# Performance work log

Hardware: AMD Instinct MI355X
Metric: run time of the kernel (lower is better)

Reference implementation:

```python
import jax, jax.numpy as jnp
import numpy as np


def _sobel_kernels(dtype):
    # kornia sobel order=1, normalized: divide by sum(|k|)=8
    gx = jnp.array([[-1., 0., 1.], [-2., 0., 2.], [-1., 0., 1.]], dtype=dtype) / 8.0
    gy = gx.T
    return jnp.stack([gx, gy])[:, None]  # (2, 1, 3, 3) OIHW


def _spatial_gradient(x):
    # x: (b, c, h, w) -> gx, gy each (b, c, h, w)
    b, c, h, w = x.shape
    xp = jnp.pad(x.reshape(b * c, 1, h, w), ((0, 0), (0, 0), (1, 1), (1, 1)), mode='edge')
    k = _sobel_kernels(x.dtype)
    out = jax.lax.conv_general_dilated(
        xp, k, window_strides=(1, 1), padding='VALID',
        dimension_numbers=('NCHW', 'OIHW', 'NCHW'))  # (b*c, 2, h, w)
    out = out.reshape(b, c, 2, h, w)
    return out[:, :, 0], out[:, :, 1]


def setup_inputs() -> dict:
    key = jax.random.key(0)
    x = jax.random.normal(key, (16, 3, 512, 512), dtype=jnp.float32)
    return {"x": x}


def reference(x):
    b, c, h, w = x.shape
    gx, gy = _spatial_gradient(x)  # (b, c, h, w) each
    if c == 3:
        mag_c = jnp.sqrt(gx * gx + gy * gy + 1e-9)  # per-channel magnitude
        # first-occurrence argmax over channels matches torch .max(dim) tie-break
        idx = jnp.argmax(mag_c, axis=1)  # (b, h, w)
        gxs = jnp.take_along_axis(gx, idx[:, None], axis=1)[:, 0]  # (b, h, w)
        gys = jnp.take_along_axis(gy, idx[:, None], axis=1)[:, 0]
    else:
        gxs, gys = gx, gy
    magnitude = jnp.sqrt(gxs * gxs + gys * gys + 1e-9)
    # clipped_div(gx, gy, 10.0)
    y_tr = jnp.where(gys == 0.0, jnp.asarray(1e-9, gys.dtype), gys)
    angle = jnp.clip(gxs / y_tr, -10.0, 10.0)
    return magnitude, angle
```

## Files before the change

### kernel.cpp

```cpp
#include <hip/hip_runtime.h>


constexpr int Hc = 512;
constexpr int Wc = 512;
constexpr int Cc = 3;

__global__ __launch_bounds__(256, 8) void sobel_mag_angle_kernel(
    const float* __restrict__ x, float* __restrict__ out, int B) {
    int tid = blockIdx.x * 256 + threadIdx.x;
    int l  = tid & 127;
    int w0 = l << 2;

    int h = __builtin_amdgcn_readfirstlane((tid >> 7) & (Hc - 1));
    int b = __builtin_amdgcn_readfirstlane(tid >> 16);
    int rm = (h == 0) ? 0 : h - 1;
    int rp = (h + 1 < Hc) ? h + 1 : Hc - 1;

    int wl = (w0 == 0) ? 0 : w0 - 1;
    int wr = (w0 + 4 < Wc) ? w0 + 4 : Wc - 1;

    const float* xb = x + (size_t)b * (Cc * Hc * Wc);

    float bm[4], bgx[4], bgy[4];

#pragma unroll
    for (int c = 0; c < Cc; ++c) {
        const float* base = xb + c * (Hc * Wc);
        const float* p0 = base + rm * Wc;
        const float* p1 = base + h * Wc;
        const float* p2 = base + rp * Wc;

        float col[3][6];
        {
            float4 v0 = *(const float4*)(p0 + w0);
            float4 v1 = *(const float4*)(p1 + w0);
            float4 v2 = *(const float4*)(p2 + w0);
            float L0 = p0[wl], R0 = p0[wr];
            float L1 = p1[wl], R1 = p1[wr];
            float L2 = p2[wl], R2 = p2[wr];
            col[0][0] = L0; col[0][1] = v0.x; col[0][2] = v0.y; col[0][3] = v0.z; col[0][4] = v0.w; col[0][5] = R0;
            col[1][0] = L1; col[1][1] = v1.x; col[1][2] = v1.y; col[1][3] = v1.z; col[1][4] = v1.w; col[1][5] = R1;
            col[2][0] = L2; col[2][1] = v2.x; col[2][2] = v2.y; col[2][3] = v2.z; col[2][4] = v2.w; col[2][5] = R2;
        }
#pragma unroll
        for (int i = 0; i < 4; ++i) {
            float t0 = col[0][i + 2] - col[0][i];
            float t1 = col[1][i + 2] - col[1][i];
            float t2 = col[2][i + 2] - col[2][i];
            float gx = 0.125f * (t0 + t2) + 0.25f * t1;
            float u0 = col[2][i]     - col[0][i];
            float u1 = col[2][i + 1] - col[0][i + 1];
            float u2 = col[2][i + 2] - col[0][i + 2];
            float gy = 0.125f * (u0 + u2) + 0.25f * u1;
            float m = __builtin_amdgcn_sqrtf(gx * gx + gy * gy + 1e-9f);
            if (c == 0) {
                bm[i] = m; bgx[i] = gx; bgy[i] = gy;
            } else {
                bool gt = m > bm[i];
                bm[i]  = gt ? m  : bm[i];
                bgx[i] = gt ? gx : bgx[i];
                bgy[i] = gt ? gy : bgy[i];
            }
        }
    }

    float mo[4], ao[4];
#pragma unroll
    for (int i = 0; i < 4; ++i) {
        mo[i] = bm[i];
        float yt = (bgy[i] == 0.0f) ? 1e-9f : bgy[i];
        float a = bgx[i] * __builtin_amdgcn_rcpf(yt);
        ao[i] = fminf(fmaxf(a, -10.0f), 10.0f);
    }

    size_t npix = (size_t)B * (Hc * Wc);
    size_t obase = ((size_t)b * Hc + h) * Wc;
    float* po = out + obase;
    *(float4*)(po + w0)        = make_float4(mo[0], mo[1], mo[2], mo[3]);
    *(float4*)(po + npix + w0) = make_float4(ao[0], ao[1], ao[2], ao[3]);
}

extern "C" void kernel_launch(void* const* d_in, const int* in_sizes, int n_in,
                              void* d_out, int out_size, void* d_ws, size_t ws_size,
                              hipStream_t stream) {
    const float* x = (const float*)d_in[0];
    float* out = (float*)d_out;
    int B = in_sizes[0] / (Cc * Hc * Wc);
    int total_threads = B * Hc * (Wc / 4);
    int blocks = total_threads / 256;
    sobel_mag_angle_kernel<<<blocks, 256, 0, stream>>>(x, out, B);
}
```

Measured before the change: 102.7 us.

## Stage row tiles with halo in LDS via direct global-to-LDS loads

Each block now covers a 4-row strip of one image. It loads 6 rows × 3 channels into shared memory with global_load_lds, so vertically adjacent output rows reuse the same input rows from LDS instead of each re-reading three rows from global memory. Each thread then computes 8 pixels of one row from LDS. The aim is to cut redundant global and L2 traffic. The cost is 36KB of LDS per block, lower occupancy, and a full wait plus barrier before any compute, with no overlap of load and compute.

```diff
diff --git a/kernel.cpp b/kernel.cpp
--- a/kernel.cpp
+++ b/kernel.cpp
@@ -1,56 +1,71 @@
 #include <hip/hip_runtime.h>
+#include <stdint.h>
 
 
 constexpr int Hc = 512;
 constexpr int Wc = 512;
 constexpr int Cc = 3;
+constexpr int RT = 4;
+constexpr int TR = RT + 2;
 
-__global__ __launch_bounds__(256, 8) void sobel_mag_angle_kernel(
+__global__ __launch_bounds__(256, 4) void sobel_mag_angle_kernel(
     const float* __restrict__ x, float* __restrict__ out, int B) {
-    int tid = blockIdx.x * 256 + threadIdx.x;
-    int l  = tid & 127;
-    int w0 = l << 2;
+    __shared__ float lds[Cc * TR * Wc];
 
-    int h = __builtin_amdgcn_readfirstlane((tid >> 7) & (Hc - 1));
-    int b = __builtin_amdgcn_readfirstlane(tid >> 16);
-    int rm = (h == 0) ? 0 : h - 1;
-    int rp = (h + 1 < Hc) ? h + 1 : Hc - 1;
+    int bid = blockIdx.x;
+    int b  = bid >> 7;
+    int h0 = (bid & 127) * RT;
 
-    int wl = (w0 == 0) ? 0 : w0 - 1;
-    int wr = (w0 + 4 < Wc) ? w0 + 4 : Wc - 1;
+    int t = threadIdx.x;
+    int wave = t >> 6;
+    int lane = t & 63;
 
     const float* xb = x + (size_t)b * (Cc * Hc * Wc);
+#pragma unroll
+    for (int s2 = 0; s2 < 9; ++s2) {
+        int s = wave * 9 + s2;
+        int ch = s / 12;
+        int rr = (s % 12) >> 1;
+        int half = s & 1;
+        int srow = h0 + rr - 1;
+        srow = srow < 0 ? 0 : (srow > Hc - 1 ? Hc - 1 : srow);
+        const float* gp = xb + ((size_t)ch * Hc + srow) * Wc + half * 256 + lane * 4;
+        float* lp = &lds[(ch * TR + rr) * Wc + half * 256];
+        __builtin_amdgcn_global_load_lds(
+            (const __attribute__((address_space(1))) void*)gp,
+            (__attribute__((address_space(3))) void*)lp, 16, 0, 0);
+    }
+    asm volatile("s_waitcnt vmcnt(0)" ::: "memory");
+    __syncthreads();
 
-    float bm[4], bgx[4], bgy[4];
+    int r = wave;
+    int w0 = lane << 3;
+    int wl = (w0 == 0) ? 0 : w0 - 1;
+    int wr = (w0 + 8 < Wc) ? w0 + 8 : Wc - 1;
 
+    float bm[8], bgx[8], bgy[8];
 #pragma unroll
     for (int c = 0; c < Cc; ++c) {
-        const float* base = xb + c * (Hc * Wc);
-        const float* p0 = base + rm * Wc;
-        const float* p1 = base + h * Wc;
-        const float* p2 = base + rp * Wc;
-
-        float col[3][6];
-        {
-            float4 v0 = *(const float4*)(p0 + w0);
-            float4 v1 = *(const float4*)(p1 + w0);
-            float4 v2 = *(const float4*)(p2 + w0);
-            float L0 = p0[wl], R0 = p0[wr];
-            float L1 = p1[wl], R1 = p1[wr];
-            float L2 = p2[wl], R2 = p2[wr];
-            col[0][0] = L0; col[0][1] = v0.x; col[0][2] = v0.y; col[0][3] = v0.z; col[0][4] = v0.w; col[0][5] = R0;
-            col[1][0] = L1; col[1][1] = v1.x; col[1][2] = v1.y; col[1][3] = v1.z; col[1][4] = v1.w; col[1][5] = R1;
-            col[2][0] = L2; col[2][1] = v2.x; col[2][2] = v2.y; col[2][3] = v2.z; col[2][4] = v2.w; col[2][5] = R2;
+        float row[3][10];
+#pragma unroll
+        for (int k = 0; k < 3; ++k) {
+            const float* lrow = &lds[(c * TR + (r + k)) * Wc];
+            float4 A  = *(const float4*)(lrow + w0);
+            float4 Bv = *(const float4*)(lrow + w0 + 4);
+            row[k][0] = lrow[wl];
+            row[k][1] = A.x;  row[k][2] = A.y;  row[k][3] = A.z;  row[k][4] = A.w;
+            row[k][5] = Bv.x; row[k][6] = Bv.y; row[k][7] = Bv.z; row[k][8] = Bv.w;
+            row[k][9] = lrow[wr];
         }
 #pragma unroll
-        for (int i = 0; i < 4; ++i) {
-            float t0 = col[0][i + 2] - col[0][i];
-            float t1 = col[1][i + 2] - col[1][i];
-            float t2 = col[2][i + 2] - col[2][i];
+        for (int i = 0; i < 8; ++i) {
+            float t0 = row[0][i + 2] - row[0][i];
+            float t1 = row[1][i + 2] - row[1][i];
+            float t2 = row[2][i + 2] - row[2][i];
             float gx = 0.125f * (t0 + t2) + 0.25f * t1;
-            float u0 = col[2][i]     - col[0][i];
-            float u1 = col[2][i + 1] - col[0][i + 1];
-            float u2 = col[2][i + 2] - col[0][i + 2];
+            float u0 = row[2][i]     - row[0][i];
+            float u1 = row[2][i + 1] - row[0][i + 1];
+            float u2 = row[2][i + 2] - row[0][i + 2];
             float gy = 0.125f * (u0 + u2) + 0.25f * u1;
             float m = __builtin_amdgcn_sqrtf(gx * gx + gy * gy + 1e-9f);
             if (c == 0) {
@@ -64,9 +79,9 @@
         }
     }
 
-    float mo[4], ao[4];
+    float mo[8], ao[8];
 #pragma unroll
-    for (int i = 0; i < 4; ++i) {
+    for (int i = 0; i < 8; ++i) {
         mo[i] = bm[i];
         float yt = (bgy[i] == 0.0f) ? 1e-9f : bgy[i];
         float a = bgx[i] * __builtin_amdgcn_rcpf(yt);
@@ -74,10 +89,12 @@
     }
 
     size_t npix = (size_t)B * (Hc * Wc);
-    size_t obase = ((size_t)b * Hc + h) * Wc;
+    size_t obase = ((size_t)b * Hc + (h0 + r)) * Wc;
     float* po = out + obase;
-    *(float4*)(po + w0)        = make_float4(mo[0], mo[1], mo[2], mo[3]);
-    *(float4*)(po + npix + w0) = make_float4(ao[0], ao[1], ao[2], ao[3]);
+    *(float4*)(po + w0)            = make_float4(mo[0], mo[1], mo[2], mo[3]);
+    *(float4*)(po + w0 + 4)        = make_float4(mo[4], mo[5], mo[6], mo[7]);
+    *(float4*)(po + npix + w0)     = make_float4(ao[0], ao[1], ao[2], ao[3]);
+    *(float4*)(po + npix + w0 + 4) = make_float4(ao[4], ao[5], ao[6], ao[7]);
 }
 
 extern "C" void kernel_launch(void* const* d_in, const int* in_sizes, int n_in,
@@ -86,7 +103,6 @@
     const float* x = (const float*)d_in[0];
     float* out = (float*)d_out;
     int B = in_sizes[0] / (Cc * Hc * Wc);
-    int total_threads = B * Hc * (Wc / 4);
-    int blocks = total_threads / 256;
+    int blocks = B * (Hc / RT);
     sobel_mag_angle_kernel<<<blocks, 256, 0, stream>>>(x, out, B);
 }
```

Result: faster. 96.31 us (-6.3%).
